# Kernel tuning notes

Hardware: AMD Instinct MI355X
Metric: run time of the kernel (lower is better)

Reference implementation:

```python
import jax, jax.numpy as jnp
import numpy as np

B, T, C, H = 2, 2048, 1024, 16
DH = C // H  # 64


def setup_inputs() -> dict:
    key = jax.random.key(0)
    ks = jax.random.split(key, 8)
    scale = 1.0 / np.sqrt(C)
    x = jax.random.normal(ks[0], (B, T, C), dtype=jnp.float32)
    mask = jax.random.randint(ks[1], (B, T), 0, 2, dtype=jnp.int32)
    Wq = jax.random.normal(ks[2], (C, C), dtype=jnp.float32) * scale
    bq = jnp.zeros((C,), dtype=jnp.float32)
    Wk = jax.random.normal(ks[3], (C, C), dtype=jnp.float32) * scale
    bk = jnp.zeros((C,), dtype=jnp.float32)
    Wv = jax.random.normal(ks[4], (C, C), dtype=jnp.float32) * scale
    bv = jnp.zeros((C,), dtype=jnp.float32)
    return {"x": x, "Wq": Wq, "bq": bq, "Wk": Wk, "bk": bk, "Wv": Wv, "bv": bv, "mask": mask}


def reference(x, Wq, bq, Wk, bk, Wv, bv, mask):
    # q/k/v projections: [B,T,C] -> [B,H,T,DH]
    def proj(W, b):
        return (x @ W + b).reshape(B, T, H, DH).transpose(0, 2, 1, 3)

    q = proj(Wq, bq)
    k = proj(Wk, bk)
    v = proj(Wv, bv)

    att = jnp.einsum("bhqd,bhkd->bhqk", q, k) * (1.0 / np.sqrt(DH))

    # outer-product padding mask: square_mask[b,q,k] = mask[b,q]*mask[b,k]
    m = mask.astype(jnp.float32)
    square_mask = m[:, :, None] * m[:, None, :]           # [B,T,T]
    sm = (square_mask != 0)[:, None, :, :]                 # [B,1,T,T]
    att = jnp.where(sm, att, -jnp.inf)

    # rows that are fully masked (query token padded) -> softmax gives NaN
    # in torch; torch then zeros the NaNs. Replicate with a safe softmax.
    row_valid = (mask != 0)[:, None, :, None]              # [B,1,T,1]
    att_safe = jnp.where(row_valid, att, 0.0)
    att = jax.nn.softmax(att_safe, axis=-1)
    att = jnp.where(row_valid, att, 0.0)
    # attn_pdrop = 0.0 -> dropout is identity

    y = jnp.einsum("bhqk,bhkd->bhqd", att, v)              # [B,H,T,DH]
    y = y.transpose(0, 2, 1, 3).reshape(B, T, C)
    return y
```

## Files before the change

kernel.cpp:

```cpp
#include <hip/hip_runtime.h>

#define B_ 2
#define T_ 2048
#define C_ 1024
#define H_ 16
#define DH_ 64

typedef __attribute__((ext_vector_type(8))) _Float16 half8;
typedef __attribute__((ext_vector_type(4))) _Float16 half4;
typedef __attribute__((ext_vector_type(2))) __fp16 fp16x2;
typedef __attribute__((ext_vector_type(4))) float f32x4;
typedef __attribute__((ext_vector_type(16))) float f32x16;

__device__ __forceinline__ unsigned short f2h(float f) {
    union { _Float16 h; unsigned short u; } cv; cv.h = (_Float16)f; return cv.u;
}
__device__ __forceinline__ unsigned pk2(float a, float b) {
    union { fp16x2 h; unsigned u; } cv;
    cv.h = __builtin_amdgcn_cvt_pkrtz(a, b);
    return cv.u;
}
__device__ __forceinline__ void plswap(unsigned &a, unsigned &b) {
    asm volatile("v_permlane32_swap_b32 %0, %1" : "+v"(a), "+v"(b));
}

__device__ __forceinline__ void gll16(const void* g, void* l) {
    __builtin_amdgcn_global_load_lds(
        (const __attribute__((address_space(1))) void*)g,
        (__attribute__((address_space(3))) void*)l, 16, 0, 0);
}

__global__ __launch_bounds__(256) void prep_kernel(
    const float* __restrict__ x, unsigned short* __restrict__ xf,
    const int* __restrict__ mask, unsigned short* __restrict__ mb,
    const float* __restrict__ Wq, const float* __restrict__ Wk,
    const float* __restrict__ Wv, unsigned short* __restrict__ wt)
{
    __shared__ float tile[32][33];
    const int tid = threadIdx.x;

    if (blockIdx.x < 2048) {
        const size_t idx8 = ((size_t)blockIdx.x * 256 + tid) * 8;
        float4 v0 = *(const float4*)(x + idx8);
        float4 v1 = *(const float4*)(x + idx8 + 4);
        float f[8] = {v0.x, v0.y, v0.z, v0.w, v1.x, v1.y, v1.z, v1.w};
        unsigned short h[8];
#pragma unroll
        for (int i = 0; i < 8; i++) h[i] = f2h(f[i]);
        *(uint4*)(xf + idx8) = *(const uint4*)h;

        if (blockIdx.x == 0) {
#pragma unroll
            for (int j = 0; j < 16; j++) {
                int i = tid * 16 + j;
                mb[i] = (mask[i] != 0) ? (unsigned short)0x3C00 : (unsigned short)0;
            }
        }
    } else {
        const int idx = blockIdx.x - 2048;
        const int z   = idx >> 10;
        const int rem = idx & 1023;
        const int n0  = (rem & 31) * 32;
        const int k0  = (rem >> 5) * 32;
        const float* __restrict__ W = (z == 0) ? Wq : (z == 1) ? Wk : Wv;
        unsigned short* __restrict__ wtz = wt + (size_t)z * C_ * C_;
        const int tx = tid & 31;
        const int ty = tid >> 5;
#pragma unroll
        for (int j = 0; j < 4; j++)
            tile[ty + j * 8][tx] = W[(size_t)(k0 + ty + j * 8) * C_ + n0 + tx];
        __syncthreads();
#pragma unroll
        for (int j = 0; j < 4; j++)
            wtz[(size_t)(n0 + ty + j * 8) * C_ + k0 + tx] = f2h(tile[tx][ty + j * 8]);
    }
}

__global__ __launch_bounds__(256) void qkv_mfma_kernel(
    const unsigned short* __restrict__ xf, const unsigned short* __restrict__ wt,
    const float* __restrict__ bq, const float* __restrict__ bk,
    const float* __restrict__ bv, const int* __restrict__ maskp,
    unsigned short* __restrict__ qb, unsigned short* __restrict__ kb,
    unsigned short* __restrict__ vt)
{
    __shared__ unsigned short sX[2][128 * 64];
    __shared__ unsigned short sW[2][128 * 64];

    const int bid  = blockIdx.x;
    const int xcd  = bid & 7;
    const int idx  = bid >> 3;
    const int tokl = idx / 12;
    const int yzl  = idx % 12;
    const int tokb = (xcd >> 1) * 8 + tokl;
    const int yz   = (xcd & 1) * 12 + yzl;
    const int z    = yz >> 3;
    const int yb   = yz & 7;

    const float* __restrict__ bias = (z == 0) ? bq : (z == 1) ? bk : bv;
    const unsigned short* __restrict__ wtz = wt + (size_t)z * C_ * C_;

    const int tok0 = tokb * 128;
    const int col0 = yb * 128;
    const int wv    = threadIdx.x >> 6;
    const int lane  = threadIdx.x & 63;
    const int l15   = lane & 15;
    const int quad  = lane >> 4;
    const int l7    = l15 & 7;
    const int wm    = wv >> 1;
    const int wn    = wv & 1;
    const int lrow8 = lane >> 3;
    const int gch   = (lane & 7) ^ lrow8;

    f32x4 acc[4][4];
#pragma unroll
    for (int i = 0; i < 4; i++)
#pragma unroll
        for (int j = 0; j < 4; j++) acc[i][j] = (f32x4){0.f, 0.f, 0.f, 0.f};

    int aoff[4][2], boff[4][2];
#pragma unroll
    for (int i = 0; i < 4; i++)
#pragma unroll
        for (int s = 0; s < 2; s++) {
            aoff[i][s] = (wm * 64 + i * 16 + l15) * 64 + (((s * 4 + quad) ^ l7) * 8);
            boff[i][s] = (wn * 64 + i * 16 + l15) * 64 + (((s * 4 + quad) ^ l7) * 8);
        }

#define STAGE_QKV(k0v, bi) do {                                               \
    _Pragma("unroll")                                                         \
    for (int s = 0; s < 8; ++s) {                                             \
        int g    = (s << 2) + wv;                                             \
        int tsel = g >> 4;                                                    \
        int r0   = (g & 15) << 3;                                             \
        const unsigned short* src = tsel ? wtz : xf;                          \
        unsigned short*       dst = tsel ? &sW[bi][0] : &sX[bi][0];           \
        int rowg = tsel ? col0 : tok0;                                        \
        gll16(src + (size_t)(rowg + r0 + lrow8) * C_ + (k0v) + gch * 8,       \
              dst + r0 * 64);                                                 \
    }                                                                         \
} while (0)

    STAGE_QKV(0, 0);

    for (int k0 = 0; k0 < C_; k0 += 64) {
        const int cur = (k0 >> 6) & 1;
        __syncthreads();
        if (k0 + 64 < C_) STAGE_QKV(k0 + 64, cur ^ 1);

        const unsigned short* Abuf = (z < 2) ? &sX[cur][0] : &sW[cur][0];
        const unsigned short* Bbuf = (z < 2) ? &sW[cur][0] : &sX[cur][0];

        half8 af[4][2], bf_[4][2];
#pragma unroll
        for (int i = 0; i < 4; i++)
#pragma unroll
            for (int s = 0; s < 2; s++) {
                af[i][s]  = *(const half8*)&Abuf[aoff[i][s]];
                bf_[i][s] = *(const half8*)&Bbuf[boff[i][s]];
            }
#pragma unroll
        for (int s = 0; s < 2; s++)
#pragma unroll
            for (int j = 0; j < 4; j++)
#pragma unroll
                for (int i = 0; i < 4; i++)
                    acc[i][j] = __builtin_amdgcn_mfma_f32_16x16x32_f16(
                        af[i][s], bf_[j][s], acc[i][j], 0, 0, 0);
    }
#undef STAGE_QKV

    if (z == 0) {
#pragma unroll
        for (int j = 0; j < 4; j++) {
            int col = col0 + wn * 64 + j * 16 + l15;
            int h = col >> 6, d = col & 63;
            float bs = bias[col];
#pragma unroll
            for (int i = 0; i < 4; i++) {
#pragma unroll
                for (int r = 0; r < 4; r++) {
                    int tok = tok0 + wm * 64 + i * 16 + quad * 4 + r;
                    int bidx = tok >> 11, t = tok & (T_ - 1);
                    qb[((size_t)(bidx * H_ + h) * T_ + t) * DH_ + d] =
                        f2h((acc[i][j][r] + bs) * 0.18033688011112042f);
                }
            }
        }
    } else if (z == 1) {
#pragma unroll
        for (int j = 0; j < 4; j++) {
            int col = col0 + wn * 64 + j * 16 + l15;
            int h = col >> 6, d = col & 63;
            float bs = bias[col];
#pragma unroll
            for (int i = 0; i < 4; i++) {
#pragma unroll
                for (int r = 0; r < 4; r++) {
                    int tok = tok0 + wm * 64 + i * 16 + quad * 4 + r;
                    int bidx = tok >> 11, t = tok & (T_ - 1);
                    kb[((size_t)(bidx * H_ + h) * T_ + t) * DH_ + d] =
                        f2h(acc[i][j][r] + bs);
                }
            }
        }
    } else {
        float mv4[4]; int bidx4[4], t4[4];
#pragma unroll
        for (int j = 0; j < 4; j++) {
            int tok = tok0 + wn * 64 + j * 16 + l15;
            bidx4[j] = tok >> 11; t4[j] = tok & (T_ - 1);
            mv4[j] = (maskp[bidx4[j] * T_ + t4[j]] != 0) ? 1.f : 0.f;
        }
#pragma unroll
        for (int i = 0; i < 4; i++) {
#pragma unroll
            for (int r = 0; r < 4; r++) {
                int col = col0 + wm * 64 + i * 16 + quad * 4 + r;
                int h = col >> 6, d = col & 63;
                float bs = bias[col];
#pragma unroll
                for (int j = 0; j < 4; j++) {
                    vt[((size_t)(bidx4[j] * H_ + h) * DH_ + d) * T_ + t4[j]] =
                        f2h((acc[i][j][r] + bs) * mv4[j]);
                }
            }
        }
    }
}

__global__ __launch_bounds__(256, 2) void attn_mfma_kernel(
    const unsigned short* __restrict__ qb,
    const unsigned short* __restrict__ kb,
    const unsigned short* __restrict__ vt,
    const int* __restrict__ mask,
    const unsigned short* __restrict__ mb,
    float* __restrict__ out)
{
    __shared__ unsigned short Ks[2][64 * 64];
    __shared__ unsigned short Vs[2][64 * 64];

    const int bh   = blockIdx.x;
    const int b    = bh >> 4;
    const int h    = bh & 15;
    const int wv   = threadIdx.x >> 6;
    const int lane = threadIdx.x & 63;
    const int l31  = lane & 31;
    const int hi   = lane >> 5;
    const int l7b  = l31 & 7;
    const int q0w  = blockIdx.y * 128 + wv * 32;

    const unsigned short* kbh = kb + (size_t)bh * T_ * DH_;
    const unsigned short* vbh = vt + (size_t)bh * DH_ * T_;
    const unsigned short* mbb = mb + b * T_;
    const int* __restrict__ mrow = mask + b * T_;

    half8 qf[4];
#pragma unroll
    for (int m = 0; m < 4; ++m)
        qf[m] = *(const half8*)(qb + ((size_t)bh * T_ + q0w + l31) * DH_
                                + m * 16 + hi * 8);

    f32x16 o0, o1, lacc;
#pragma unroll
    for (int r = 0; r < 16; ++r) { o0[r] = 0.f; o1[r] = 0.f; lacc[r] = 0.f; }

    const int lrow = lane >> 3;
    const int gch  = (lane & 7) ^ lrow;

#pragma unroll
    for (int s = 0; s < 4; ++s) {
        int j  = (wv << 2) + s;
        int rb = j & 7;
        if (j < 8) gll16(kbh + (size_t)(rb * 8 + lrow) * DH_ + gch * 8, &Ks[0][rb * 512]);
        else       gll16(vbh + (size_t)(rb * 8 + lrow) * T_  + gch * 8, &Vs[0][rb * 512]);
    }

    for (int kt = 0; kt < 32; ++kt) {
        const int cur   = kt & 1;
        const int kbase = kt * 64;
        __syncthreads();

        if (kt < 31) {
            const int nb = kbase + 64;
#pragma unroll
            for (int s = 0; s < 4; ++s) {
                int j  = (wv << 2) + s;
                int rb = j & 7;
                if (j < 8) gll16(kbh + (size_t)(nb + rb * 8 + lrow) * DH_ + gch * 8,
                                 &Ks[cur ^ 1][rb * 512]);
                else       gll16(vbh + (size_t)(rb * 8 + lrow) * T_ + nb + gch * 8,
                                 &Vs[cur ^ 1][rb * 512]);
            }
        }

        const unsigned short* Kc = &Ks[cur][0];
        const unsigned short* Vc = &Vs[cur][0];

        half8 bm[4];
#pragma unroll
        for (int c = 0; c < 4; ++c)
            bm[c] = *(const half8*)(mbb + kbase + c * 16 + hi * 8);

        half8 pa[4];
#pragma unroll
        for (int st = 0; st < 2; ++st) {
            f32x16 sa;
#pragma unroll
            for (int r = 0; r < 16; ++r) sa[r] = 0.f;
#pragma unroll
            for (int m = 0; m < 4; ++m) {
                half8 kf = *(const half8*)(Kc + (st * 32 + l31) * 64
                                           + (((m * 2 + hi) ^ l7b) * 8));
                sa = __builtin_amdgcn_mfma_f32_32x32x16_f16(kf, qf[m], sa, 0, 0, 0);
            }
            float p[16];
#pragma unroll
            for (int r = 0; r < 16; ++r) p[r] = __builtin_amdgcn_exp2f(sa[r]);
#pragma unroll
            for (int kh = 0; kh < 2; ++kh) {
                unsigned w0 = pk2(p[kh * 8 + 0], p[kh * 8 + 1]);
                unsigned w2 = pk2(p[kh * 8 + 4], p[kh * 8 + 5]);
                unsigned w1 = pk2(p[kh * 8 + 2], p[kh * 8 + 3]);
                unsigned w3 = pk2(p[kh * 8 + 6], p[kh * 8 + 7]);
                plswap(w0, w2);
                plswap(w1, w3);
                union { unsigned u[4]; half8 hh; } cv;
                cv.u[0] = w0; cv.u[1] = w1; cv.u[2] = w2; cv.u[3] = w3;
                pa[st * 2 + kh] = cv.hh;
            }
        }

#pragma unroll
        for (int c = 0; c < 4; ++c)
            lacc = __builtin_amdgcn_mfma_f32_32x32x16_f16(pa[c], bm[c], lacc, 0, 0, 0);

#pragma unroll
        for (int c = 0; c < 4; ++c) {
            half8 v0 = *(const half8*)(Vc + (l31) * 64      + (((c * 2 + hi) ^ l7b) * 8));
            half8 v1 = *(const half8*)(Vc + (32 + l31) * 64 + (((c * 2 + hi) ^ l7b) * 8));
            o0 = __builtin_amdgcn_mfma_f32_32x32x16_f16(pa[c], v0, o0, 0, 0, 0);
            o1 = __builtin_amdgcn_mfma_f32_32x32x16_f16(pa[c], v1, o1, 0, 0, 0);
        }
    }

#pragma unroll
    for (int r = 0; r < 16; ++r) {
        int q = q0w + (r & 3) + 8 * (r >> 2) + 4 * hi;
        float lv = lacc[r];
        float iv = (mrow[q] != 0 && lv > 0.f) ? (1.0f / lv) : 0.f;
        float* orow = out + ((size_t)(b * T_ + q)) * C_ + h * DH_;
        orow[l31]      = o0[r] * iv;
        orow[32 + l31] = o1[r] * iv;
    }
}

extern "C" void kernel_launch(void* const* d_in, const int* in_sizes, int n_in,
                              void* d_out, int out_size, void* d_ws, size_t ws_size,
                              hipStream_t stream)
{
    (void)in_sizes; (void)n_in; (void)out_size; (void)ws_size;
    const float* x  = (const float*)d_in[0];
    const float* Wq = (const float*)d_in[1];
    const float* bq = (const float*)d_in[2];
    const float* Wk = (const float*)d_in[3];
    const float* bk = (const float*)d_in[4];
    const float* Wv = (const float*)d_in[5];
    const float* bv = (const float*)d_in[6];
    const int* mask = (const int*)d_in[7];
    float* out = (float*)d_out;

    const size_t NX = (size_t)B_ * T_ * C_;
    unsigned short* xf = (unsigned short*)d_ws;
    unsigned short* wt = xf + NX;
    unsigned short* qb = wt + (size_t)3 * C_ * C_;
    unsigned short* kb = qb + NX;
    unsigned short* vt = kb + NX;
    unsigned short* mb = vt + NX;

    prep_kernel<<<5120, 256, 0, stream>>>(x, xf, mask, mb, Wq, Wk, Wv, wt);
    qkv_mfma_kernel<<<768, 256, 0, stream>>>(
        xf, wt, bq, bk, bv, mask, qb, kb, vt);
    attn_mfma_kernel<<<dim3(32, 16), 256, 0, stream>>>(qb, kb, vt, mask, mb, out);
}
```

Measured before the change: 167.3 us.

## Software-pipeline attention loop: overlap QK of next tile with PV of current

Restructures the attention main loop so each step computes QK^T and the exp for tile kt+1 while doing the P·V and row-sum MFMAs for tile kt, with K prefetched two tiles ahead and V one tile ahead. The loop is unrolled by two with ping-pong P register buffers and a prologue and epilogue. The goal is to give the scheduler independent MFMA and exp work to interleave and to hide LDS and global load latency. The cost is higher register pressure from the two P buffers and more complex buffer indexing.

```diff
diff --git a/kernel.cpp b/kernel.cpp
--- a/kernel.cpp
+++ b/kernel.cpp
@@ -267,81 +267,97 @@
     const int lrow = lane >> 3;
     const int gch  = (lane & 7) ^ lrow;
 
+#define QK_BLOCK(KRDp, PA) do {                                               \
+    _Pragma("unroll")                                                         \
+    for (int st = 0; st < 2; ++st) {                                          \
+        f32x16 sa;                                                            \
+        _Pragma("unroll") for (int r = 0; r < 16; ++r) sa[r] = 0.f;           \
+        _Pragma("unroll") for (int m = 0; m < 4; ++m) {                       \
+            half8 kf = *(const half8*)((KRDp) + (st * 32 + l31) * 64          \
+                                       + (((m * 2 + hi) ^ l7b) * 8));         \
+            sa = __builtin_amdgcn_mfma_f32_32x32x16_f16(kf, qf[m], sa, 0,0,0);\
+        }                                                                     \
+        float p[16];                                                          \
+        _Pragma("unroll") for (int r = 0; r < 16; ++r)                        \
+            p[r] = __builtin_amdgcn_exp2f(sa[r]);                             \
+        _Pragma("unroll") for (int kh = 0; kh < 2; ++kh) {                    \
+            unsigned w0 = pk2(p[kh * 8 + 0], p[kh * 8 + 1]);                  \
+            unsigned w2 = pk2(p[kh * 8 + 4], p[kh * 8 + 5]);                  \
+            unsigned w1 = pk2(p[kh * 8 + 2], p[kh * 8 + 3]);                  \
+            unsigned w3 = pk2(p[kh * 8 + 6], p[kh * 8 + 7]);                  \
+            plswap(w0, w2);                                                   \
+            plswap(w1, w3);                                                   \
+            union { unsigned u[4]; half8 hh; } cv;                            \
+            cv.u[0] = w0; cv.u[1] = w1; cv.u[2] = w2; cv.u[3] = w3;           \
+            (PA)[st * 2 + kh] = cv.hh;                                        \
+        }                                                                     \
+    }                                                                         \
+} while (0)
+
+#define PV_BLOCK(KT, VRDp, PAC) do {                                          \
+    half8 bmx[4];                                                             \
+    _Pragma("unroll") for (int c = 0; c < 4; ++c)                             \
+        bmx[c] = *(const half8*)(mbb + (KT) * 64 + c * 16 + hi * 8);          \
+    _Pragma("unroll") for (int c = 0; c < 4; ++c)                             \
+        lacc = __builtin_amdgcn_mfma_f32_32x32x16_f16((PAC)[c], bmx[c],       \
+                                                      lacc, 0, 0, 0);         \
+    _Pragma("unroll") for (int c = 0; c < 4; ++c) {                           \
+        half8 v0 = *(const half8*)((VRDp) + (l31) * 64                        \
+                                   + (((c * 2 + hi) ^ l7b) * 8));             \
+        half8 v1 = *(const half8*)((VRDp) + (32 + l31) * 64                   \
+                                   + (((c * 2 + hi) ^ l7b) * 8));             \
+        o0 = __builtin_amdgcn_mfma_f32_32x32x16_f16((PAC)[c], v0, o0, 0,0,0); \
+        o1 = __builtin_amdgcn_mfma_f32_32x32x16_f16((PAC)[c], v1, o1, 0,0,0); \
+    }                                                                         \
+} while (0)
+
+#define ATTN_STEP(KT, KD, KR, VD, VR, PAC, PAN, DOK) do {                     \
+    __syncthreads();                                                          \
+    {                                                                         \
+        const int nbk = ((KT) + 2) * 64, nbv = ((KT) + 1) * 64;               \
+        _Pragma("unroll") for (int s = 0; s < 4; ++s) {                       \
+            int j = (wv << 2) + s, rb = j & 7;                                \
+            if (j < 8) {                                                      \
+                if (DOK) gll16(kbh + (size_t)(nbk + rb * 8 + lrow) * DH_      \
+                               + gch * 8, &(KD)[rb * 512]);                   \
+            } else {                                                          \
+                gll16(vbh + (size_t)(rb * 8 + lrow) * T_ + nbv + gch * 8,     \
+                      &(VD)[rb * 512]);                                       \
+            }                                                                 \
+        }                                                                     \
+    }                                                                         \
+    QK_BLOCK(&(KR)[0], PAN);                                                  \
+    PV_BLOCK(KT, &(VR)[0], PAC);                                              \
+} while (0)
+
 #pragma unroll
     for (int s = 0; s < 4; ++s) {
-        int j  = (wv << 2) + s;
-        int rb = j & 7;
+        int j = (wv << 2) + s, rb = j & 7;
         if (j < 8) gll16(kbh + (size_t)(rb * 8 + lrow) * DH_ + gch * 8, &Ks[0][rb * 512]);
         else       gll16(vbh + (size_t)(rb * 8 + lrow) * T_  + gch * 8, &Vs[0][rb * 512]);
     }
-
-    for (int kt = 0; kt < 32; ++kt) {
-        const int cur   = kt & 1;
-        const int kbase = kt * 64;
-        __syncthreads();
-
-        if (kt < 31) {
-            const int nb = kbase + 64;
-#pragma unroll
-            for (int s = 0; s < 4; ++s) {
-                int j  = (wv << 2) + s;
-                int rb = j & 7;
-                if (j < 8) gll16(kbh + (size_t)(nb + rb * 8 + lrow) * DH_ + gch * 8,
-                                 &Ks[cur ^ 1][rb * 512]);
-                else       gll16(vbh + (size_t)(rb * 8 + lrow) * T_ + nb + gch * 8,
-                                 &Vs[cur ^ 1][rb * 512]);
-            }
-        }
-
-        const unsigned short* Kc = &Ks[cur][0];
-        const unsigned short* Vc = &Vs[cur][0];
-
-        half8 bm[4];
-#pragma unroll
-        for (int c = 0; c < 4; ++c)
-            bm[c] = *(const half8*)(mbb + kbase + c * 16 + hi * 8);
-
-        half8 pa[4];
-#pragma unroll
-        for (int st = 0; st < 2; ++st) {
-            f32x16 sa;
-#pragma unroll
-            for (int r = 0; r < 16; ++r) sa[r] = 0.f;
-#pragma unroll
-            for (int m = 0; m < 4; ++m) {
-                half8 kf = *(const half8*)(Kc + (st * 32 + l31) * 64
-                                           + (((m * 2 + hi) ^ l7b) * 8));
-                sa = __builtin_amdgcn_mfma_f32_32x32x16_f16(kf, qf[m], sa, 0, 0, 0);
-            }
-            float p[16];
-#pragma unroll
-            for (int r = 0; r < 16; ++r) p[r] = __builtin_amdgcn_exp2f(sa[r]);
-#pragma unroll
-            for (int kh = 0; kh < 2; ++kh) {
-                unsigned w0 = pk2(p[kh * 8 + 0], p[kh * 8 + 1]);
-                unsigned w2 = pk2(p[kh * 8 + 4], p[kh * 8 + 5]);
-                unsigned w1 = pk2(p[kh * 8 + 2], p[kh * 8 + 3]);
-                unsigned w3 = pk2(p[kh * 8 + 6], p[kh * 8 + 7]);
-                plswap(w0, w2);
-                plswap(w1, w3);
-                union { unsigned u[4]; half8 hh; } cv;
-                cv.u[0] = w0; cv.u[1] = w1; cv.u[2] = w2; cv.u[3] = w3;
-                pa[st * 2 + kh] = cv.hh;
-            }
-        }
-
-#pragma unroll
-        for (int c = 0; c < 4; ++c)
-            lacc = __builtin_amdgcn_mfma_f32_32x32x16_f16(pa[c], bm[c], lacc, 0, 0, 0);
-
-#pragma unroll
-        for (int c = 0; c < 4; ++c) {
-            half8 v0 = *(const half8*)(Vc + (l31) * 64      + (((c * 2 + hi) ^ l7b) * 8));
-            half8 v1 = *(const half8*)(Vc + (32 + l31) * 64 + (((c * 2 + hi) ^ l7b) * 8));
-            o0 = __builtin_amdgcn_mfma_f32_32x32x16_f16(pa[c], v0, o0, 0, 0, 0);
-            o1 = __builtin_amdgcn_mfma_f32_32x32x16_f16(pa[c], v1, o1, 0, 0, 0);
-        }
-    }
+#pragma unroll
+    for (int s = 0; s < 2; ++s) {
+        int rb = (wv << 1) + s;
+        gll16(kbh + (size_t)(64 + rb * 8 + lrow) * DH_ + gch * 8, &Ks[1][rb * 512]);
+    }
+    __syncthreads();
+
+    half8 paA[4], paB[4];
+    QK_BLOCK(&Ks[0][0], paA);
+
+    for (int kt = 0; kt < 30; kt += 2) {
+        ATTN_STEP(kt,     Ks[0], Ks[1], Vs[1], Vs[0], paA, paB, true);
+        ATTN_STEP(kt + 1, Ks[1], Ks[0], Vs[0], Vs[1], paB, paA, true);
+    }
+    ATTN_STEP(30, Ks[0], Ks[1], Vs[1], Vs[0], paA, paB, false);
+
+    __syncthreads();
+    PV_BLOCK(31, &Vs[1][0], paB);
+
+#undef ATTN_STEP
+#undef PV_BLOCK
+#undef QK_BLOCK
 
 #pragma unroll
     for (int r = 0; r < 16; ++r) {
```

After: 168.3 us, median of 3. Within noise of the previous version (+0.6%).

## Triple-buffer X tiles in QKV GEMM with split staging and partial vmcnt waits

Applied to the files above, without the earlier changes.

Splits the QKV projection's global-to-LDS staging into separate X and W loads. X gets a three-deep ring buffer so it is prefetched two k-steps ahead, while W stays double-buffered. The full barrier wait is replaced by an explicit s_waitcnt vmcnt(4) plus s_barrier, which lets later loads remain in flight during compute. The aim is to hide more global load latency, at the cost of extra LDS use (which may lower occupancy) and reliance on correct manual vmcnt accounting.

```diff
diff --git a/kernel.cpp b/kernel.cpp
--- a/kernel.cpp
+++ b/kernel.cpp
@@ -83,7 +83,7 @@
     unsigned short* __restrict__ qb, unsigned short* __restrict__ kb,
     unsigned short* __restrict__ vt)
 {
-    __shared__ unsigned short sX[2][128 * 64];
+    __shared__ unsigned short sX[3][128 * 64];
     __shared__ unsigned short sW[2][128 * 64];
 
     const int bid  = blockIdx.x;
@@ -126,48 +126,64 @@
             boff[i][s] = (wn * 64 + i * 16 + l15) * 64 + (((s * 4 + quad) ^ l7) * 8);
         }
 
-#define STAGE_QKV(k0v, bi) do {                                               \
+#define STAGE_X(k0v, bi) do {                                                 \
     _Pragma("unroll")                                                         \
-    for (int s = 0; s < 8; ++s) {                                             \
-        int g    = (s << 2) + wv;                                             \
-        int tsel = g >> 4;                                                    \
-        int r0   = (g & 15) << 3;                                             \
-        const unsigned short* src = tsel ? wtz : xf;                          \
-        unsigned short*       dst = tsel ? &sW[bi][0] : &sX[bi][0];           \
-        int rowg = tsel ? col0 : tok0;                                        \
-        gll16(src + (size_t)(rowg + r0 + lrow8) * C_ + (k0v) + gch * 8,       \
-              dst + r0 * 64);                                                 \
+    for (int s = 0; s < 4; ++s) {                                             \
+        int g  = (s << 2) + wv;                                               \
+        int r0 = g << 3;                                                      \
+        gll16(xf + (size_t)(tok0 + r0 + lrow8) * C_ + (k0v) + gch * 8,        \
+              &sX[bi][r0 * 64]);                                              \
     }                                                                         \
 } while (0)
-
-    STAGE_QKV(0, 0);
-
-    for (int k0 = 0; k0 < C_; k0 += 64) {
-        const int cur = (k0 >> 6) & 1;
-        __syncthreads();
-        if (k0 + 64 < C_) STAGE_QKV(k0 + 64, cur ^ 1);
-
-        const unsigned short* Abuf = (z < 2) ? &sX[cur][0] : &sW[cur][0];
-        const unsigned short* Bbuf = (z < 2) ? &sW[cur][0] : &sX[cur][0];
-
-        half8 af[4][2], bf_[4][2];
-#pragma unroll
-        for (int i = 0; i < 4; i++)
-#pragma unroll
-            for (int s = 0; s < 2; s++) {
-                af[i][s]  = *(const half8*)&Abuf[aoff[i][s]];
-                bf_[i][s] = *(const half8*)&Bbuf[boff[i][s]];
-            }
-#pragma unroll
-        for (int s = 0; s < 2; s++)
-#pragma unroll
-            for (int j = 0; j < 4; j++)
-#pragma unroll
-                for (int i = 0; i < 4; i++)
-                    acc[i][j] = __builtin_amdgcn_mfma_f32_16x16x32_f16(
-                        af[i][s], bf_[j][s], acc[i][j], 0, 0, 0);
-    }
-#undef STAGE_QKV
+#define STAGE_W(k0v, bi) do {                                                 \
+    _Pragma("unroll")                                                         \
+    for (int s = 0; s < 4; ++s) {                                             \
+        int g  = (s << 2) + wv;                                               \
+        int r0 = g << 3;                                                      \
+        gll16(wtz + (size_t)(col0 + r0 + lrow8) * C_ + (k0v) + gch * 8,       \
+              &sW[bi][r0 * 64]);                                              \
+    }                                                                         \
+} while (0)
+
+#define QKV_COMPUTE(T) do {                                                   \
+    const unsigned short* Xc = &sX[(T) % 3][0];                               \
+    const unsigned short* Wc = &sW[(T) & 1][0];                               \
+    const unsigned short* Abuf = (z < 2) ? Xc : Wc;                           \
+    const unsigned short* Bbuf = (z < 2) ? Wc : Xc;                           \
+    half8 af[4][2], bf_[4][2];                                                \
+    _Pragma("unroll")                                                         \
+    for (int i = 0; i < 4; i++)                                               \
+        _Pragma("unroll")                                                     \
+        for (int s = 0; s < 2; s++) {                                         \
+            af[i][s]  = *(const half8*)&Abuf[aoff[i][s]];                     \
+            bf_[i][s] = *(const half8*)&Bbuf[boff[i][s]];                     \
+        }                                                                     \
+    _Pragma("unroll")                                                         \
+    for (int s = 0; s < 2; s++)                                               \
+        _Pragma("unroll")                                                     \
+        for (int j = 0; j < 4; j++)                                           \
+            _Pragma("unroll")                                                 \
+            for (int i = 0; i < 4; i++)                                       \
+                acc[i][j] = __builtin_amdgcn_mfma_f32_16x16x32_f16(           \
+                    af[i][s], bf_[j][s], acc[i][j], 0, 0, 0);                 \
+} while (0)
+
+    STAGE_X(0, 0);
+    STAGE_W(0, 0);
+    STAGE_X(64, 1);
+
+    for (int t = 0; t < 15; ++t) {
+        asm volatile("s_waitcnt vmcnt(4)\n\ts_barrier" ::: "memory");
+        STAGE_W((t + 1) * 64, (t + 1) & 1);
+        if (t + 2 < 16) STAGE_X((t + 2) * 64, (t + 2) % 3);
+        QKV_COMPUTE(t);
+    }
+    asm volatile("s_waitcnt vmcnt(0)\n\ts_barrier" ::: "memory");
+    QKV_COMPUTE(15);
+
+#undef QKV_COMPUTE
+#undef STAGE_W
+#undef STAGE_X
 
     if (z == 0) {
 #pragma unroll
```

New measurement: 174.0 us. +4.0%, slower.

## Process two 32-query tiles per wave to reuse K/V fragments

Applied to the files above, without the earlier changes.

Each wave in the attention kernel now computes 64 query rows as two 32-row sub-tiles. K fragments loaded from LDS feed both sub-tiles, and V fragments feed the PV MFMAs for both. This halves LDS traffic and K/V staging per query. The grid is halved, and launch bounds drop to one block per SIMD group to allow the doubled accumulator registers, which reduces occupancy and the number of blocks available to fill the CUs.

```diff
diff --git a/kernel.cpp b/kernel.cpp
--- a/kernel.cpp
+++ b/kernel.cpp
@@ -228,7 +228,7 @@
     }
 }
 
-__global__ __launch_bounds__(256, 2) void attn_mfma_kernel(
+__global__ __launch_bounds__(256, 1) void attn_mfma_kernel(
     const unsigned short* __restrict__ qb,
     const unsigned short* __restrict__ kb,
     const unsigned short* __restrict__ vt,
@@ -247,22 +247,27 @@
     const int l31  = lane & 31;
     const int hi   = lane >> 5;
     const int l7b  = l31 & 7;
-    const int q0w  = blockIdx.y * 128 + wv * 32;
+    const int q0w  = blockIdx.y * 256 + wv * 64;
 
     const unsigned short* kbh = kb + (size_t)bh * T_ * DH_;
     const unsigned short* vbh = vt + (size_t)bh * DH_ * T_;
     const unsigned short* mbb = mb + b * T_;
     const int* __restrict__ mrow = mask + b * T_;
 
-    half8 qf[4];
-#pragma unroll
-    for (int m = 0; m < 4; ++m)
-        qf[m] = *(const half8*)(qb + ((size_t)bh * T_ + q0w + l31) * DH_
-                                + m * 16 + hi * 8);
-
-    f32x16 o0, o1, lacc;
-#pragma unroll
-    for (int r = 0; r < 16; ++r) { o0[r] = 0.f; o1[r] = 0.f; lacc[r] = 0.f; }
+    half8 qf[2][4];
+#pragma unroll
+    for (int qn = 0; qn < 2; ++qn)
+#pragma unroll
+        for (int m = 0; m < 4; ++m)
+            qf[qn][m] = *(const half8*)(qb + ((size_t)bh * T_ + q0w + qn * 32 + l31) * DH_
+                                        + m * 16 + hi * 8);
+
+    f32x16 o[2][2], lacc[2];
+#pragma unroll
+    for (int qn = 0; qn < 2; ++qn) {
+#pragma unroll
+        for (int r = 0; r < 16; ++r) { o[qn][0][r] = 0.f; o[qn][1][r] = 0.f; lacc[qn][r] = 0.f; }
+    }
 
     const int lrow = lane >> 3;
     const int gch  = (lane & 7) ^ lrow;
@@ -301,56 +306,70 @@
         for (int c = 0; c < 4; ++c)
             bm[c] = *(const half8*)(mbb + kbase + c * 16 + hi * 8);
 
-        half8 pa[4];
+        half8 pa[2][4];
 #pragma unroll
         for (int st = 0; st < 2; ++st) {
-            f32x16 sa;
-#pragma unroll
-            for (int r = 0; r < 16; ++r) sa[r] = 0.f;
-#pragma unroll
-            for (int m = 0; m < 4; ++m) {
-                half8 kf = *(const half8*)(Kc + (st * 32 + l31) * 64
-                                           + (((m * 2 + hi) ^ l7b) * 8));
-                sa = __builtin_amdgcn_mfma_f32_32x32x16_f16(kf, qf[m], sa, 0, 0, 0);
-            }
-            float p[16];
-#pragma unroll
-            for (int r = 0; r < 16; ++r) p[r] = __builtin_amdgcn_exp2f(sa[r]);
-#pragma unroll
-            for (int kh = 0; kh < 2; ++kh) {
-                unsigned w0 = pk2(p[kh * 8 + 0], p[kh * 8 + 1]);
-                unsigned w2 = pk2(p[kh * 8 + 4], p[kh * 8 + 5]);
-                unsigned w1 = pk2(p[kh * 8 + 2], p[kh * 8 + 3]);
-                unsigned w3 = pk2(p[kh * 8 + 6], p[kh * 8 + 7]);
-                plswap(w0, w2);
-                plswap(w1, w3);
-                union { unsigned u[4]; half8 hh; } cv;
-                cv.u[0] = w0; cv.u[1] = w1; cv.u[2] = w2; cv.u[3] = w3;
-                pa[st * 2 + kh] = cv.hh;
-            }
-        }
-
-#pragma unroll
-        for (int c = 0; c < 4; ++c)
-            lacc = __builtin_amdgcn_mfma_f32_32x32x16_f16(pa[c], bm[c], lacc, 0, 0, 0);
+            half8 kf[4];
+#pragma unroll
+            for (int m = 0; m < 4; ++m)
+                kf[m] = *(const half8*)(Kc + (st * 32 + l31) * 64
+                                        + (((m * 2 + hi) ^ l7b) * 8));
+#pragma unroll
+            for (int qn = 0; qn < 2; ++qn) {
+                f32x16 sa;
+#pragma unroll
+                for (int r = 0; r < 16; ++r) sa[r] = 0.f;
+#pragma unroll
+                for (int m = 0; m < 4; ++m)
+                    sa = __builtin_amdgcn_mfma_f32_32x32x16_f16(kf[m], qf[qn][m], sa, 0, 0, 0);
+                float p[16];
+#pragma unroll
+                for (int r = 0; r < 16; ++r) p[r] = __builtin_amdgcn_exp2f(sa[r]);
+#pragma unroll
+                for (int kh = 0; kh < 2; ++kh) {
+                    unsigned w0 = pk2(p[kh * 8 + 0], p[kh * 8 + 1]);
+                    unsigned w2 = pk2(p[kh * 8 + 4], p[kh * 8 + 5]);
+                    unsigned w1 = pk2(p[kh * 8 + 2], p[kh * 8 + 3]);
+                    unsigned w3 = pk2(p[kh * 8 + 6], p[kh * 8 + 7]);
+                    plswap(w0, w2);
+                    plswap(w1, w3);
+                    union { unsigned u[4]; half8 hh; } cv;
+                    cv.u[0] = w0; cv.u[1] = w1; cv.u[2] = w2; cv.u[3] = w3;
+                    pa[qn][st * 2 + kh] = cv.hh;
+                }
+            }
+        }
+
+#pragma unroll
+        for (int qn = 0; qn < 2; ++qn)
+#pragma unroll
+            for (int c = 0; c < 4; ++c)
+                lacc[qn] = __builtin_amdgcn_mfma_f32_32x32x16_f16(pa[qn][c], bm[c],
+                                                                  lacc[qn], 0, 0, 0);
 
 #pragma unroll
         for (int c = 0; c < 4; ++c) {
             half8 v0 = *(const half8*)(Vc + (l31) * 64      + (((c * 2 + hi) ^ l7b) * 8));
             half8 v1 = *(const half8*)(Vc + (32 + l31) * 64 + (((c * 2 + hi) ^ l7b) * 8));
-            o0 = __builtin_amdgcn_mfma_f32_32x32x16_f16(pa[c], v0, o0, 0, 0, 0);
-            o1 = __builtin_amdgcn_mfma_f32_32x32x16_f16(pa[c], v1, o1, 0, 0, 0);
-        }
-    }
-
-#pragma unroll
-    for (int r = 0; r < 16; ++r) {
-        int q = q0w + (r & 3) + 8 * (r >> 2) + 4 * hi;
-        float lv = lacc[r];
-        float iv = (mrow[q] != 0 && lv > 0.f) ? (1.0f / lv) : 0.f;
-        float* orow = out + ((size_t)(b * T_ + q)) * C_ + h * DH_;
-        orow[l31]      = o0[r] * iv;
-        orow[32 + l31] = o1[r] * iv;
+#pragma unroll
+            for (int qn = 0; qn < 2; ++qn) {
+                o[qn][0] = __builtin_amdgcn_mfma_f32_32x32x16_f16(pa[qn][c], v0, o[qn][0], 0, 0, 0);
+                o[qn][1] = __builtin_amdgcn_mfma_f32_32x32x16_f16(pa[qn][c], v1, o[qn][1], 0, 0, 0);
+            }
+        }
+    }
+
+#pragma unroll
+    for (int qn = 0; qn < 2; ++qn) {
+#pragma unroll
+        for (int r = 0; r < 16; ++r) {
+            int q = q0w + qn * 32 + (r & 3) + 8 * (r >> 2) + 4 * hi;
+            float lv = lacc[qn][r];
+            float iv = (mrow[q] != 0 && lv > 0.f) ? (1.0f / lv) : 0.f;
+            float* orow = out + ((size_t)(b * T_ + q)) * C_ + h * DH_;
+            orow[l31]      = o[qn][0][r] * iv;
+            orow[32 + l31] = o[qn][1][r] * iv;
+        }
     }
 }
 
@@ -380,5 +399,5 @@
     prep_kernel<<<5120, 256, 0, stream>>>(x, xf, mask, mb, Wq, Wk, Wv, wt);
     qkv_mfma_kernel<<<768, 256, 0, stream>>>(
         xf, wt, bq, bk, bv, mask, qb, kb, vt);
-    attn_mfma_kernel<<<dim3(32, 16), 256, 0, stream>>>(qb, kb, vt, mask, mb, out);
-}
+    attn_mfma_kernel<<<dim3(32, 8), 256, 0, stream>>>(qb, kb, vt, mask, mb, out);
+}
```

After: 175.6 us. +5.0%, slower.
